# Optimization experiments

Hardware: AMD Instinct MI355X
Metric: run time of the kernel (lower is better)

Reference implementation:

```python
import jax, jax.numpy as jnp
import numpy as np

N_NODES = 10000
NEG_SLOPE_ATT = 0.5   # GATConv negative_slope
NEG_SLOPE_ACT = 0.01  # F.leaky_relu default used as self.act


def setup_inputs() -> dict:
    key = jax.random.key(0)
    k1, k2, k3, k4, k5 = jax.random.split(key, 5)
    in_dim, out_dim = 512, 128
    x = jax.random.normal(k1, (N_NODES, in_dim), dtype=jnp.float32)
    edge_index = jax.random.randint(k2, (2, 320000), 0, N_NODES, dtype=jnp.int64)
    # glorot-ish scaled params
    W = jax.random.normal(k3, (in_dim, out_dim), dtype=jnp.float32) * (1.0 / np.sqrt(in_dim))
    att_src = jax.random.normal(k4, (out_dim,), dtype=jnp.float32) * (1.0 / np.sqrt(out_dim))
    att_dst = jax.random.normal(k5, (out_dim,), dtype=jnp.float32) * (1.0 / np.sqrt(out_dim))
    bias = jnp.zeros((out_dim,), dtype=jnp.float32)
    return {"x": x, "edge_index": edge_index, "W": W,
            "att_src": att_src, "att_dst": att_dst, "bias": bias}


def _leaky(v, slope):
    return jnp.where(v >= 0, v, slope * v)


def reference(x, edge_index, W, att_src, att_dst, bias):
    N = x.shape[0]
    loop = jnp.arange(N, dtype=edge_index.dtype)
    src = jnp.concatenate([edge_index[0], loop])  # message source j
    dst = jnp.concatenate([edge_index[1], loop])  # message target i

    h = x @ W                      # [N, out_dim]
    a_src = h @ att_src            # [N]
    a_dst = h @ att_dst            # [N]

    e = _leaky(a_src[src] + a_dst[dst], NEG_SLOPE_ATT)   # [E+N]
    # segment softmax over incoming edges of each dst node
    m = jax.ops.segment_max(e, dst, num_segments=N)
    ex = jnp.exp(e - m[dst])
    denom = jax.ops.segment_sum(ex, dst, num_segments=N)
    alpha = ex / denom[dst]

    out = jax.ops.segment_sum(h[src] * alpha[:, None], dst, num_segments=N) + bias
    embed_x = _leaky(out, NEG_SLOPE_ACT)                 # self.act = F.leaky_relu
    recon = jax.nn.sigmoid(embed_x @ embed_x.T)          # [N, N]
    return recon, embed_x
```

## Files before the change

kernel.cpp:

```cpp
#include <hip/hip_runtime.h>
#include <stdint.h>
#include <math.h>


typedef __attribute__((ext_vector_type(8))) short short8v;
typedef __attribute__((ext_vector_type(4))) float f32x4;

#define IN_DIM 512
#define OUT_DIM 128
#define NEG_ATT 0.5f
#define NEG_ACT 0.01f

__device__ __forceinline__ float leakyf(float v, float s) { return v >= 0.f ? v : s * v; }

__device__ __forceinline__ uint16_t f2bf(float v) {
  uint32_t u = __float_as_uint(v);
  u += 0x7FFFu + ((u >> 16) & 1u);
  return (uint16_t)(u >> 16);
}
__device__ __forceinline__ float bf2f(uint16_t b) { return __uint_as_float(((uint32_t)b) << 16); }

__global__ __launch_bounds__(256) void k_h_gemm(const float* __restrict__ x,
                                                const float* __restrict__ W,
                                                const float* __restrict__ att_s_g,
                                                const float* __restrict__ att_d_g,
                                                const int* __restrict__ e_dst,
                                                int* __restrict__ cnt, int E,
                                                uint16_t* __restrict__ h16,
                                                float* __restrict__ a_src,
                                                float* __restrict__ a_dst, int N) {
  int tid = threadIdx.x;
  int tx = tid & 31, ty = tid >> 5;
  int row0 = blockIdx.x * 16 + ty * 2;
  int rc[2];
  #pragma unroll
  for (int r = 0; r < 2; ++r) rc[r] = (row0 + r < N) ? (row0 + r) : (N - 1);

  f32x4 acc[2];
  #pragma unroll
  for (int r = 0; r < 2; ++r) acc[r] = (f32x4){0.f, 0.f, 0.f, 0.f};

  for (int k = 0; k < IN_DIM; k += 4) {
    f32x4 wreg[4];
    #pragma unroll
    for (int kk = 0; kk < 4; ++kk)
      wreg[kk] = *(const f32x4*)&W[(size_t)(k + kk) * OUT_DIM + tx * 4];
    #pragma unroll
    for (int r = 0; r < 2; ++r) {
      f32x4 xv = *(const f32x4*)&x[(size_t)rc[r] * IN_DIM + k];
      #pragma unroll
      for (int kk = 0; kk < 4; ++kk) {
        acc[r][0] = fmaf(xv[kk], wreg[kk][0], acc[r][0]);
        acc[r][1] = fmaf(xv[kk], wreg[kk][1], acc[r][1]);
        acc[r][2] = fmaf(xv[kk], wreg[kk][2], acc[r][2]);
        acc[r][3] = fmaf(xv[kk], wreg[kk][3], acc[r][3]);
      }
    }
  }

  float atts[4], attd[4];
  #pragma unroll
  for (int j = 0; j < 4; ++j) { atts[j] = att_s_g[tx * 4 + j]; attd[j] = att_d_g[tx * 4 + j]; }
  #pragma unroll
  for (int r = 0; r < 2; ++r) {
    int row = row0 + r;
    float ps = 0.f, pd = 0.f;
    #pragma unroll
    for (int j = 0; j < 4; ++j) { ps = fmaf(acc[r][j], atts[j], ps); pd = fmaf(acc[r][j], attd[j], pd); }
    #pragma unroll
    for (int off = 16; off; off >>= 1) {
      ps += __shfl_xor(ps, off);
      pd += __shfl_xor(pd, off);
    }
    if (row < N) {
      uint32_t lo = (uint32_t)f2bf(acc[r][0]) | ((uint32_t)f2bf(acc[r][1]) << 16);
      uint32_t hi = (uint32_t)f2bf(acc[r][2]) | ((uint32_t)f2bf(acc[r][3]) << 16);
      uint2 pk; pk.x = lo; pk.y = hi;
      *(uint2*)&h16[(size_t)row * OUT_DIM + tx * 4] = pk;
      if (tx == 0) { a_src[row] = ps; a_dst[row] = pd; }
    }
  }

  int e0 = blockIdx.x * 512 + tid;
  if (e0 < E) atomicAdd(&cnt[e_dst[e0]], 1);
  int e1 = e0 + 256;
  if (e1 < E) atomicAdd(&cnt[e_dst[e1]], 1);
}

__global__ __launch_bounds__(1024) void k_scan(const int* __restrict__ cnt,
                                               int* __restrict__ row_start,
                                               int* __restrict__ cursor, int N) {
  __shared__ int sd[1024];
  int t = threadIdx.x;
  const int CH = (N + 1023) >> 10;
  int base = t * CH;
  int s = 0;
  for (int k = 0; k < CH; ++k) { int i = base + k; if (i < N) s += cnt[i]; }
  sd[t] = s;
  __syncthreads();
  for (int off = 1; off < 1024; off <<= 1) {
    int v = (t >= off) ? sd[t - off] : 0;
    __syncthreads();
    sd[t] += v;
    __syncthreads();
  }
  int run = (t == 0) ? 0 : sd[t - 1];
  for (int k = 0; k < CH; ++k) {
    int i = base + k;
    if (i < N) { row_start[i] = run; cursor[i] = run; run += cnt[i]; }
  }
  if (t == 1023) row_start[N] = sd[1023];
}
__global__ void k_fill(const int* __restrict__ src, const int* __restrict__ dst,
                       int* __restrict__ cursor, int* __restrict__ csr, int E) {
  int e = blockIdx.x * blockDim.x + threadIdx.x;
  if (e < E) {
    int d = dst[e];
    int pos = atomicAdd(&cursor[d], 1);
    csr[pos] = src[e];
  }
}

__global__ __launch_bounds__(256) void k_aggregate(
    const uint16_t* __restrict__ h16, const float* __restrict__ a_src,
    const float* __restrict__ a_dst, const int* __restrict__ row_start,
    const int* __restrict__ csr, const float* __restrict__ bias,
    float* __restrict__ embed_out, uint16_t* __restrict__ ebf, int N, int NPAD) {
  int wid = (int)((blockIdx.x * blockDim.x + threadIdx.x) >> 6);
  int lane = threadIdx.x & 63;
  if (wid >= N) {
    if (wid < NPAD) {
      ebf[(size_t)wid * OUT_DIM + lane] = 0;
      ebf[(size_t)wid * OUT_DIM + 64 + lane] = 0;
    }
    return;
  }
  int i = wid;
  int s0 = row_start[i], s1 = row_start[i + 1];
  float adst = a_dst[i];
  float eself = leakyf(a_src[i] + adst, NEG_ATT);
  float m = eself;
  for (int k = s0 + lane; k < s1; k += 64) {
    float e = leakyf(a_src[csr[k]] + adst, NEG_ATT);
    m = fmaxf(m, e);
  }
  #pragma unroll
  for (int off = 32; off; off >>= 1) m = fmaxf(m, __shfl_xor(m, off));
  float dsum = 0.f;
  for (int k = s0 + lane; k < s1; k += 64) {
    float e = leakyf(a_src[csr[k]] + adst, NEG_ATT);
    dsum += __expf(e - m);
  }
  #pragma unroll
  for (int off = 32; off; off >>= 1) dsum += __shfl_xor(dsum, off);
  dsum += __expf(eself - m);
  float inv = 1.0f / dsum;
  float wself = __expf(eself - m) * inv;
  float acc0 = bf2f(h16[(size_t)i * OUT_DIM + lane]) * wself;
  float acc1 = bf2f(h16[(size_t)i * OUT_DIM + 64 + lane]) * wself;
  #pragma unroll 4
  for (int k = s0; k < s1; ++k) {
    int s = csr[k];
    float w = __expf(leakyf(a_src[s] + adst, NEG_ATT) - m) * inv;
    acc0 = fmaf(bf2f(h16[(size_t)s * OUT_DIM + lane]), w, acc0);
    acc1 = fmaf(bf2f(h16[(size_t)s * OUT_DIM + 64 + lane]), w, acc1);
  }
  float o0 = leakyf(acc0 + bias[lane], NEG_ACT);
  float o1 = leakyf(acc1 + bias[64 + lane], NEG_ACT);
  embed_out[(size_t)i * OUT_DIM + lane] = o0;
  embed_out[(size_t)i * OUT_DIM + 64 + lane] = o1;
  ebf[(size_t)i * OUT_DIM + lane] = f2bf(o0);
  ebf[(size_t)i * OUT_DIM + 64 + lane] = f2bf(o1);
}

__global__ __launch_bounds__(512, 4) void k_recon(const uint16_t* __restrict__ ebf,
                                                  float* __restrict__ out,
                                                  int N, int nb) {
  __shared__ __align__(16) unsigned char smem[65536];
  uint16_t* sA = (uint16_t*)smem;
  uint16_t* sB = (uint16_t*)(smem + 32768);
  float* sO = (float*)smem;

  int tid = threadIdx.x;
  int wid = tid >> 6, lane = tid & 63;
  int wr = wid >> 2, wc = wid & 3;
  int r16 = lane & 15, kg = lane >> 4;

  int NT = nb * (nb + 1) / 2;
  int q = NT >> 3, r8 = NT & 7;
  int orig = blockIdx.x;
  int xcd = orig & 7, sub = orig >> 3;
  int k = (xcd < r8 ? xcd * (q + 1) : r8 * (q + 1) + (xcd - r8) * q) + sub;
  int by = (int)((2.0 * nb + 1.0 -
                  sqrt((2.0 * nb + 1.0) * (2.0 * nb + 1.0) - 8.0 * (double)k)) * 0.5);
  if (by < 0) by = 0;
  if (by > nb - 1) by = nb - 1;
  while ((by + 1) * nb - ((by + 1) * by) / 2 <= k) ++by;
  while (by * nb - (by * (by - 1)) / 2 > k) --by;
  int bx = by + (k - (by * nb - (by * (by - 1)) / 2));
  int rowBlk = by * 128, colBlk = bx * 128;

  #pragma unroll
  for (int p = 0; p < 4; ++p) {
    int i2 = p * 512 + tid;
    int row = i2 >> 4, slot = i2 & 15;
    f32x4 va = *(const f32x4*)&ebf[(size_t)(rowBlk + row) * OUT_DIM + slot * 8];
    f32x4 vb = *(const f32x4*)&ebf[(size_t)(colBlk + row) * OUT_DIM + slot * 8];
    int ss = slot ^ (row & 7);
    *(f32x4*)&sA[row * OUT_DIM + ss * 8] = va;
    *(f32x4*)&sB[row * OUT_DIM + ss * 8] = vb;
  }
  __syncthreads();

  int rowWl = wr * 64, colWl = wc * 32;
  f32x4 acc[4][2];
  #pragma unroll
  for (int a = 0; a < 4; ++a)
    #pragma unroll
    for (int b = 0; b < 2; ++b) acc[a][b] = (f32x4){0.f, 0.f, 0.f, 0.f};

  #pragma unroll
  for (int kc = 0; kc < 4; ++kc) {
    short8v bfr[2];
    #pragma unroll
    for (int tj = 0; tj < 2; ++tj) {
      int rw = colWl + tj * 16 + r16;
      int ss = (kc * 4 + kg) ^ (rw & 7);
      bfr[tj] = *(const short8v*)&sB[rw * OUT_DIM + ss * 8];
    }
    #pragma unroll
    for (int ti = 0; ti < 4; ++ti) {
      int rw = rowWl + ti * 16 + r16;
      int ss = (kc * 4 + kg) ^ (rw & 7);
      short8v af = *(const short8v*)&sA[rw * OUT_DIM + ss * 8];
      #pragma unroll
      for (int tj = 0; tj < 2; ++tj)
        acc[ti][tj] = __builtin_amdgcn_mfma_f32_16x16x32_bf16(af, bfr[tj], acc[ti][tj], 0, 0, 0);
    }
  }
  __syncthreads();

  #pragma unroll
  for (int ti = 0; ti < 4; ++ti)
    #pragma unroll
    for (int tj = 0; tj < 2; ++tj) {
      int c = colWl + tj * 16 + r16;
      #pragma unroll
      for (int qq = 0; qq < 4; ++qq) {
        int r = rowWl + ti * 16 + kg * 4 + qq;
        float sg = 1.0f / (1.0f + __expf(-acc[ti][tj][qq]));
        sO[r * 128 + (c ^ r)] = sg;
      }
    }
  __syncthreads();

  bool colFull = (colBlk + 128 <= N);
  #pragma unroll
  for (int p = 0; p < 8; ++p) {
    int i2 = p * 512 + tid;
    int row = i2 >> 5, cg = (i2 & 31) * 4;
    int rr = rowBlk + row;
    if (rr < N) {
      f32x4 v;
      #pragma unroll
      for (int j = 0; j < 4; ++j) v[j] = sO[row * 128 + ((cg + j) ^ row)];
      int col = colBlk + cg;
      if (colFull) {
        __builtin_nontemporal_store(v, (f32x4*)&out[(size_t)rr * N + col]);
      } else {
        #pragma unroll
        for (int j = 0; j < 4; ++j)
          if (col + j < N) __builtin_nontemporal_store(v[j], &out[(size_t)rr * N + col + j]);
      }
    }
  }

  if (by != bx) {
    #pragma unroll
    for (int p = 0; p < 8; ++p) {
      int i2 = p * 512 + tid;
      int u = i2 >> 5, cg = (i2 & 31) * 4;
      int rr = colBlk + u;
      if (rr < N) {
        f32x4 v;
        #pragma unroll
        for (int j = 0; j < 4; ++j) v[j] = sO[(cg + j) * 128 + (u ^ (cg + j))];
        __builtin_nontemporal_store(v, (f32x4*)&out[(size_t)rr * N + rowBlk + cg]);
      }
    }
  }
}

extern "C" void kernel_launch(void* const* d_in, const int* in_sizes, int n_in,
                              void* d_out, int out_size, void* d_ws, size_t ws_size,
                              hipStream_t stream) {
  const float* x = (const float*)d_in[0];
  const int* ei = (const int*)d_in[1];
  const float* W = (const float*)d_in[2];
  const float* att_s = (const float*)d_in[3];
  const float* att_d = (const float*)d_in[4];
  const float* bias = (const float*)d_in[5];

  const int N = in_sizes[0] / IN_DIM;
  const int E = in_sizes[1] / 2;
  const int NB = (N + 127) / 128;
  const int NPAD = NB * 128;

  float* out = (float*)d_out;
  float* embed_out = out + (size_t)N * N;

  uint16_t* h16 = (uint16_t*)d_ws;
  float* a_src = (float*)(h16 + (size_t)N * OUT_DIM);
  float* a_dst = a_src + N;
  int* cnt = (int*)(a_dst + N);
  int* row_start = cnt + N;
  int* cursor = row_start + (N + 4);
  int* csr = cursor + N;
  uint16_t* ebf = (uint16_t*)(csr + E);

  const int* e_src = ei;
  const int* e_dst = ei + E;

  hipMemsetAsync(cnt, 0, (size_t)N * sizeof(int), stream);
  k_h_gemm<<<dim3((N + 15) / 16), 256, 0, stream>>>(x, W, att_s, att_d,
                                                    e_dst, cnt, E, h16, a_src, a_dst, N);
  k_scan<<<dim3(1), 1024, 0, stream>>>(cnt, row_start, cursor, N);
  k_fill<<<dim3((E + 255) / 256), 256, 0, stream>>>(e_src, e_dst, cursor, csr, E);
  k_aggregate<<<dim3((NPAD * 64 + 255) / 256), 256, 0, stream>>>(
      h16, a_src, a_dst, row_start, csr, bias, embed_out, ebf, N, NPAD);
  const int NT = NB * (NB + 1) / 2;
  k_recon<<<dim3(NT), 512, 0, stream>>>(ebf, out, N, NB);
}
```

Measured before the change: 230.0 us.

## Restructure recon as 16-row slabs sweeping column strips, dropping symmetric tiling

Replaces the symmetric upper-triangular 128x128 tile scheme, which wrote each off-diagonal tile twice (once transposed), with a row-slab scheme. Each block owns 16 rows and half the column strips, keeps its row fragments in registers, and streams column strips through LDS. Output stores become contiguous row segments instead of transposed writes. In exchange it computes the full N×N product rather than half, reloads column strips per slab, and adds two barriers per strip. It also assumes N is divisible by 16.

```diff
diff --git a/kernel.cpp b/kernel.cpp
--- a/kernel.cpp
+++ b/kernel.cpp
@@ -1,6 +1,5 @@
 #include <hip/hip_runtime.h>
 #include <stdint.h>
-#include <math.h>
 
 
 typedef __attribute__((ext_vector_type(8))) short short8v;
@@ -173,119 +172,69 @@
   ebf[(size_t)i * OUT_DIM + 64 + lane] = f2bf(o1);
 }
 
-__global__ __launch_bounds__(512, 4) void k_recon(const uint16_t* __restrict__ ebf,
+__global__ __launch_bounds__(256, 4) void k_recon(const uint16_t* __restrict__ ebf,
                                                   float* __restrict__ out,
-                                                  int N, int nb) {
-  __shared__ __align__(16) unsigned char smem[65536];
-  uint16_t* sA = (uint16_t*)smem;
-  uint16_t* sB = (uint16_t*)(smem + 32768);
-  float* sO = (float*)smem;
+                                                  int N, int nStrips) {
+  __shared__ __align__(16) uint16_t sB[128 * OUT_DIM];
+  __shared__ __align__(16) float sO[16 * 132];
 
   int tid = threadIdx.x;
   int wid = tid >> 6, lane = tid & 63;
-  int wr = wid >> 2, wc = wid & 3;
   int r16 = lane & 15, kg = lane >> 4;
 
-  int NT = nb * (nb + 1) / 2;
-  int q = NT >> 3, r8 = NT & 7;
-  int orig = blockIdx.x;
-  int xcd = orig & 7, sub = orig >> 3;
-  int k = (xcd < r8 ? xcd * (q + 1) : r8 * (q + 1) + (xcd - r8) * q) + sub;
-  int by = (int)((2.0 * nb + 1.0 -
-                  sqrt((2.0 * nb + 1.0) * (2.0 * nb + 1.0) - 8.0 * (double)k)) * 0.5);
-  if (by < 0) by = 0;
-  if (by > nb - 1) by = nb - 1;
-  while ((by + 1) * nb - ((by + 1) * by) / 2 <= k) ++by;
-  while (by * nb - (by * (by - 1)) / 2 > k) --by;
-  int bx = by + (k - (by * nb - (by * (by - 1)) / 2));
-  int rowBlk = by * 128, colBlk = bx * 128;
-
-  #pragma unroll
-  for (int p = 0; p < 4; ++p) {
-    int i2 = p * 512 + tid;
-    int row = i2 >> 4, slot = i2 & 15;
-    f32x4 va = *(const f32x4*)&ebf[(size_t)(rowBlk + row) * OUT_DIM + slot * 8];
-    f32x4 vb = *(const f32x4*)&ebf[(size_t)(colBlk + row) * OUT_DIM + slot * 8];
-    int ss = slot ^ (row & 7);
-    *(f32x4*)&sA[row * OUT_DIM + ss * 8] = va;
-    *(f32x4*)&sB[row * OUT_DIM + ss * 8] = vb;
-  }
-  __syncthreads();
-
-  int rowWl = wr * 64, colWl = wc * 32;
-  f32x4 acc[4][2];
-  #pragma unroll
-  for (int a = 0; a < 4; ++a)
-    #pragma unroll
-    for (int b = 0; b < 2; ++b) acc[a][b] = (f32x4){0.f, 0.f, 0.f, 0.f};
-
-  #pragma unroll
-  for (int kc = 0; kc < 4; ++kc) {
-    short8v bfr[2];
-    #pragma unroll
-    for (int tj = 0; tj < 2; ++tj) {
-      int rw = colWl + tj * 16 + r16;
-      int ss = (kc * 4 + kg) ^ (rw & 7);
-      bfr[tj] = *(const short8v*)&sB[rw * OUT_DIM + ss * 8];
-    }
-    #pragma unroll
-    for (int ti = 0; ti < 4; ++ti) {
-      int rw = rowWl + ti * 16 + r16;
-      int ss = (kc * 4 + kg) ^ (rw & 7);
-      short8v af = *(const short8v*)&sA[rw * OUT_DIM + ss * 8];
+  int slab = blockIdx.x >> 1;
+  int half = blockIdx.x & 1;
+  int rowBase = slab * 16;
+  int sH = nStrips >> 1;
+  int strip0 = half ? (nStrips - sH) : 0;
+  int strip1 = half ? nStrips : (nStrips - sH);
+
+  short8v rowfrag[4];
+  #pragma unroll
+  for (int kc = 0; kc < 4; ++kc)
+    rowfrag[kc] = *(const short8v*)&ebf[(size_t)(rowBase + r16) * OUT_DIM + kc * 32 + kg * 8];
+
+  for (int strip = strip0; strip < strip1; ++strip) {
+    int colBase = strip * 128;
+    #pragma unroll
+    for (int p = 0; p < 8; ++p) {
+      int i2 = p * 256 + tid;
+      int row = i2 >> 4, slot = i2 & 15;
+      f32x4 vb = *(const f32x4*)&ebf[(size_t)(colBase + row) * OUT_DIM + slot * 8];
+      int ss = slot ^ (row & 7);
+      *(f32x4*)&sB[row * OUT_DIM + ss * 8] = vb;
+    }
+    __syncthreads();
+    #pragma unroll
+    for (int tt = 0; tt < 2; ++tt) {
+      int t = wid * 2 + tt;
+      f32x4 acc = (f32x4){0.f, 0.f, 0.f, 0.f};
       #pragma unroll
-      for (int tj = 0; tj < 2; ++tj)
-        acc[ti][tj] = __builtin_amdgcn_mfma_f32_16x16x32_bf16(af, bfr[tj], acc[ti][tj], 0, 0, 0);
-    }
-  }
-  __syncthreads();
-
-  #pragma unroll
-  for (int ti = 0; ti < 4; ++ti)
-    #pragma unroll
-    for (int tj = 0; tj < 2; ++tj) {
-      int c = colWl + tj * 16 + r16;
+      for (int kc = 0; kc < 4; ++kc) {
+        int cn = t * 16 + r16;
+        int ss = (kc * 4 + kg) ^ (cn & 7);
+        short8v cf = *(const short8v*)&sB[cn * OUT_DIM + ss * 8];
+        acc = __builtin_amdgcn_mfma_f32_16x16x32_bf16(cf, rowfrag[kc], acc, 0, 0, 0);
+      }
+      f32x4 sg;
       #pragma unroll
-      for (int qq = 0; qq < 4; ++qq) {
-        int r = rowWl + ti * 16 + kg * 4 + qq;
-        float sg = 1.0f / (1.0f + __expf(-acc[ti][tj][qq]));
-        sO[r * 128 + (c ^ r)] = sg;
-      }
-    }
-  __syncthreads();
-
-  bool colFull = (colBlk + 128 <= N);
-  #pragma unroll
-  for (int p = 0; p < 8; ++p) {
-    int i2 = p * 512 + tid;
-    int row = i2 >> 5, cg = (i2 & 31) * 4;
-    int rr = rowBlk + row;
-    if (rr < N) {
-      f32x4 v;
-      #pragma unroll
-      for (int j = 0; j < 4; ++j) v[j] = sO[row * 128 + ((cg + j) ^ row)];
-      int col = colBlk + cg;
-      if (colFull) {
-        __builtin_nontemporal_store(v, (f32x4*)&out[(size_t)rr * N + col]);
+      for (int q = 0; q < 4; ++q) sg[q] = 1.0f / (1.0f + __expf(-acc[q]));
+      *(f32x4*)&sO[r16 * 132 + t * 16 + kg * 4] = sg;
+    }
+    __syncthreads();
+    #pragma unroll
+    for (int it = 0; it < 2; ++it) {
+      int row = it * 8 + (tid >> 5);
+      int c4 = tid & 31;
+      f32x4 v = *(const f32x4*)&sO[row * 132 + c4 * 4];
+      int col = colBase + c4 * 4;
+      size_t o = (size_t)(rowBase + row) * N + col;
+      if (col + 3 < N) {
+        __builtin_nontemporal_store(v, (f32x4*)&out[o]);
       } else {
         #pragma unroll
         for (int j = 0; j < 4; ++j)
-          if (col + j < N) __builtin_nontemporal_store(v[j], &out[(size_t)rr * N + col + j]);
-      }
-    }
-  }
-
-  if (by != bx) {
-    #pragma unroll
-    for (int p = 0; p < 8; ++p) {
-      int i2 = p * 512 + tid;
-      int u = i2 >> 5, cg = (i2 & 31) * 4;
-      int rr = colBlk + u;
-      if (rr < N) {
-        f32x4 v;
-        #pragma unroll
-        for (int j = 0; j < 4; ++j) v[j] = sO[(cg + j) * 128 + (u ^ (cg + j))];
-        __builtin_nontemporal_store(v, (f32x4*)&out[(size_t)rr * N + rowBlk + cg]);
+          if (col + j < N) __builtin_nontemporal_store(v[j], &out[o + j]);
       }
     }
   }
@@ -328,6 +277,6 @@
   k_fill<<<dim3((E + 255) / 256), 256, 0, stream>>>(e_src, e_dst, cursor, csr, E);
   k_aggregate<<<dim3((NPAD * 64 + 255) / 256), 256, 0, stream>>>(
       h16, a_src, a_dst, row_start, csr, bias, embed_out, ebf, N, NPAD);
-  const int NT = NB * (NB + 1) / 2;
-  k_recon<<<dim3(NT), 512, 0, stream>>>(ebf, out, N, NB);
-}
+  const int nSlabs = N / 16;
+  k_recon<<<dim3(nSlabs * 2), 256, 0, stream>>>(ebf, out, N, NB);
+}
```

New measurement: 250.2 us. +8.8%, slower.
